# Kernel tuning notes

Measured on AMD Instinct MI355X. Metric: run time of the kernel, lower is better.

The kernel has to match this reference:

```python
import jax, jax.numpy as jnp
import numpy as np
from jax import lax

B, T, E, H, V, D_ACT, OUT = 128, 512, 12, 512, 16, 10, 64


def setup_inputs() -> dict:
    key = jax.random.key(0)
    ks = jax.random.split(key, 9)
    ts = jax.random.uniform(ks[0], (B, T, 2), dtype=jnp.float32)
    idx = jax.random.randint(ks[1], (B, T), 0, V).astype(jnp.float32)
    x = jnp.concatenate([ts, idx[..., None]], axis=-1)  # [B,T,3], col2 = activity ids
    emb = jax.random.normal(ks[2], (V, D_ACT), jnp.float32) * 0.1
    emb = emb.at[0].set(0.0)  # padding_idx=0
    W_fwd = jax.random.normal(ks[3], (E, 3 * H), jnp.float32) / np.sqrt(E).astype(np.float32)
    b_fwd = jnp.zeros((3 * H,), jnp.float32)
    W_bwd = jax.random.normal(ks[4], (E, 3 * H), jnp.float32) / np.sqrt(E).astype(np.float32)
    b_bwd = jnp.zeros((3 * H,), jnp.float32)
    weight_Mu = jax.random.normal(ks[5], (2 * H, 1), jnp.float32) * 0.1
    W_out = jax.random.normal(ks[6], (OUT, 2 * H), jnp.float32) * 0.01  # torch Linear layout [out,in]
    b_out = jnp.zeros((OUT,), jnp.float32)
    return {"x": x, "emb": emb, "W_fwd": W_fwd, "b_fwd": b_fwd,
            "W_bwd": W_bwd, "b_bwd": b_bwd, "weight_Mu": weight_Mu,
            "W_out": W_out, "b_out": b_out}


def _fo_pool(z, f):
    # h_t = f_t * h_{t-1} + (1 - f_t) * z_t, scanned over time (axis 0)
    def step(c, zf):
        z_t, f_t = zf
        c = f_t * c + (1.0 - f_t) * z_t
        return c, c
    c0 = jnp.zeros_like(z[0])
    _, cs = lax.scan(step, c0, (z, f))
    return cs  # [T,B,H]


def _qrnn_dir(inp, W, b):
    # inp: [T,B,E] -> gates [T,B,3H]
    Y = inp @ W + b
    Z, F_, O = jnp.split(Y, 3, axis=-1)
    Z = jnp.tanh(Z)
    F_ = jax.nn.sigmoid(F_)
    O = jax.nn.sigmoid(O)
    C = _fo_pool(Z, F_)
    return O * C  # [T,B,H]


def reference(x, emb, W_fwd, b_fwd, W_bwd, b_bwd, weight_Mu, W_out, b_out):
    ts = x[:, :, :2]                                   # [B,T,2] time features
    act = emb[x[:, :, 2].astype(jnp.int32)]            # [B,T,10]
    enc = jnp.concatenate([ts, act], axis=-1)          # [B,T,E]
    inp = jnp.transpose(enc, (1, 0, 2))                # [T,B,E]
    h_f = _qrnn_dir(inp, W_fwd, b_fwd)                 # [T,B,H]
    h_b = _qrnn_dir(inp[::-1], W_bwd, b_bwd)[::-1]     # reverse-direction QRNN
    out = jnp.concatenate([h_f, h_b], axis=-1)         # [T,B,2H]
    out = jax.nn.relu(jnp.transpose(out, (1, 0, 2)))   # [B,T,2H]
    attn = jax.nn.softmax(out @ weight_Mu, axis=1)     # [B,T,1], softmax over time
    context = jnp.einsum('btd,bt->bd', out, attn[..., 0])  # [B,2H]
    context = jax.nn.relu(context)
    return context @ W_out.T + b_out                   # [B,OUT]
```

## Files before the change

kernel.cpp:

```cpp
#include <hip/hip_runtime.h>
#include <hip/hip_bf16.h>

#define B_   128
#define T_   512
#define H_   512
#define V_   16
#define OUT_ 64
#define DH_  1024

#define TAB_BYTES (V_*H_*16)
#define TSA_BYTES (T_*8)
#define VPK_BYTES (T_)
#define SCAN_LDS  (TAB_BYTES + TSA_BYTES + VPK_BYTES)

__device__ __forceinline__ float bf2f(unsigned short u) {
    union { unsigned int i; float f; } x; x.i = ((unsigned int)u) << 16; return x.f;
}

__global__ __launch_bounds__(256) void zero_kernel(float4* __restrict__ p, int n4)
{
    const int i = blockIdx.x * 256 + threadIdx.x;
    if (i < n4) p[i] = make_float4(0.f, 0.f, 0.f, 0.f);
}

__global__ __launch_bounds__(512) void qrnn_scan4(
    const float* __restrict__ x,
    const float* __restrict__ emb,
    const float* __restrict__ Wf, const float* __restrict__ bf_,
    const float* __restrict__ Wb, const float* __restrict__ bb_,
    __hip_bfloat16* __restrict__ hbuf)
{
    const int b = blockIdx.x, dir = blockIdx.y, h = threadIdx.x;
    const float* __restrict__ W    = dir ? Wb  : Wf;
    const float* __restrict__ bias = dir ? bb_ : bf_;

    extern __shared__ char smem[];
    float4*        tab = (float4*)smem;
    float2*        tsA = (float2*)(smem + TAB_BYTES);
    unsigned char* vpk = (unsigned char*)(smem + TAB_BYTES + TSA_BYTES);

    {
        const int t = h;
        const float* xp = x + ((size_t)b*T_ + t)*3;
        tsA[t] = make_float2(xp[0], xp[1]);
        vpk[t] = (unsigned char)(int)xp[2];
    }

    float w0[3], w1[3], wt[10][3];
#pragma unroll
    for (int g = 0; g < 3; ++g) {
        w0[g] = W[g*H_ + h];
        w1[g] = W[1536 + g*H_ + h];
#pragma unroll
        for (int e = 0; e < 10; ++e)
            wt[e][g] = W[(2+e)*1536 + g*H_ + h];
    }
    const float bz = bias[h], bfv = bias[H_+h], bov = bias[2*H_+h];

    const float FZ = -2.8853900817779268f;
    const float FF = -1.4426950408889634f;

#pragma unroll
    for (int v = 0; v < V_; ++v) {
        float a0 = bz, a1 = bfv, a2 = bov;
#pragma unroll
        for (int e = 0; e < 10; ++e) {
            const float ev = emb[v*10 + e];
            a0 = fmaf(ev, wt[e][0], a0);
            a1 = fmaf(ev, wt[e][1], a1);
            a2 = fmaf(ev, wt[e][2], a2);
        }
        tab[v*H_ + h] = make_float4(FZ*a0, FF*a1, FF*a2, 0.f);
    }
    const float w0z = FZ*w0[0], w0f = FF*w0[1], w0o = FF*w0[2];
    const float w1z = FZ*w1[0], w1f = FF*w1[1], w1o = FF*w1[2];
    __syncthreads();

    const float4* tsA4 = (const float4*)tsA;
    const uint2*  vp2  = (const uint2*)vpk;

    float c = 0.f;
    __hip_bfloat16* hb = hbuf + (size_t)b*T_*DH_ + dir*H_ + h;

#define STEP(i, TS0, TS1, G) { \
    const int t = t0 + (i); \
    const float zp = fmaf(TS0, w0z, fmaf(TS1, w1z, (G).x)); \
    const float fp = fmaf(TS0, w0f, fmaf(TS1, w1f, (G).y)); \
    const float op = fmaf(TS0, w0o, fmaf(TS1, w1o, (G).z)); \
    const float rz = __builtin_amdgcn_rcpf(1.f + __builtin_amdgcn_exp2f(zp)); \
    const float f  = __builtin_amdgcn_rcpf(1.f + __builtin_amdgcn_exp2f(fp)); \
    const float o  = __builtin_amdgcn_rcpf(1.f + __builtin_amdgcn_exp2f(op)); \
    const float z  = fmaf(2.f, rz, -1.f); \
    c = fmaf(f, c - z, z); \
    const float hv = fmaxf(o * c, 0.f); \
    hb[(size_t)t*DH_] = __float2bfloat16(hv); \
}

#pragma unroll 2
    for (int gi = 0; gi < T_/8; ++gi) {
        const int gg = dir ? (T_/8 - 1 - gi) : gi;
        const int t0 = gg*8;
        const uint2  vp  = vp2[gg];
        const float4 tsa = tsA4[gg*4 + 0];
        const float4 tsb = tsA4[gg*4 + 1];
        const float4 tsc = tsA4[gg*4 + 2];
        const float4 tsd = tsA4[gg*4 + 3];
        const int v0 =  vp.x        & 255, v1 = (vp.x >> 8) & 255;
        const int v2 = (vp.x >> 16) & 255, v3 =  vp.x >> 24;
        const int v4 =  vp.y        & 255, v5 = (vp.y >> 8) & 255;
        const int v6 = (vp.y >> 16) & 255, v7 =  vp.y >> 24;
        const float4 g0 = tab[v0*H_ + h];
        const float4 g1 = tab[v1*H_ + h];
        const float4 g2 = tab[v2*H_ + h];
        const float4 g3 = tab[v3*H_ + h];
        const float4 g4 = tab[v4*H_ + h];
        const float4 g5 = tab[v5*H_ + h];
        const float4 g6 = tab[v6*H_ + h];
        const float4 g7 = tab[v7*H_ + h];
        if (dir == 0) {
            STEP(0, tsa.x, tsa.y, g0) STEP(1, tsa.z, tsa.w, g1)
            STEP(2, tsb.x, tsb.y, g2) STEP(3, tsb.z, tsb.w, g3)
            STEP(4, tsc.x, tsc.y, g4) STEP(5, tsc.z, tsc.w, g5)
            STEP(6, tsd.x, tsd.y, g6) STEP(7, tsd.z, tsd.w, g7)
        } else {
            STEP(7, tsd.z, tsd.w, g7) STEP(6, tsd.x, tsd.y, g6)
            STEP(5, tsc.z, tsc.w, g5) STEP(4, tsc.x, tsc.y, g4)
            STEP(3, tsb.z, tsb.w, g3) STEP(2, tsb.x, tsb.y, g2)
            STEP(1, tsa.z, tsa.w, g1) STEP(0, tsa.x, tsa.y, g0)
        }
    }
#undef STEP
}

__global__ __launch_bounds__(256) void score2(
    const __hip_bfloat16* __restrict__ hbuf, const float* __restrict__ Mu,
    float* __restrict__ s)
{
    const int row  = blockIdx.x*4 + (threadIdx.x >> 6);
    const int lane = threadIdx.x & 63;
    const uint4* hp = (const uint4*)(hbuf + (size_t)row*DH_);
    const float4* mp = (const float4*)Mu;
    float acc = 0.f;
#pragma unroll
    for (int k = 0; k < 2; ++k) {
        const int idx = k*64 + lane;
        const uint4 hv = hp[idx];
        const float4 m0 = mp[idx*2];
        const float4 m1 = mp[idx*2 + 1];
        acc = fmaf(bf2f((unsigned short)(hv.x & 0xffffu)), m0.x, acc);
        acc = fmaf(bf2f((unsigned short)(hv.x >> 16)),     m0.y, acc);
        acc = fmaf(bf2f((unsigned short)(hv.y & 0xffffu)), m0.z, acc);
        acc = fmaf(bf2f((unsigned short)(hv.y >> 16)),     m0.w, acc);
        acc = fmaf(bf2f((unsigned short)(hv.z & 0xffffu)), m1.x, acc);
        acc = fmaf(bf2f((unsigned short)(hv.z >> 16)),     m1.y, acc);
        acc = fmaf(bf2f((unsigned short)(hv.w & 0xffffu)), m1.z, acc);
        acc = fmaf(bf2f((unsigned short)(hv.w >> 16)),     m1.w, acc);
    }
#pragma unroll
    for (int off = 32; off; off >>= 1) acc += __shfl_down(acc, off);
    if (lane == 0) s[row] = acc;
}

__global__ __launch_bounds__(512) void softmax_kernel(
    const float* __restrict__ s, float* __restrict__ w)
{
    const int b = blockIdx.x;
    const int t = threadIdx.x;
    const float v = s[b*T_ + t];

    __shared__ float redm[8];
    __shared__ float reds[8];

    float m = v;
#pragma unroll
    for (int off = 32; off; off >>= 1) m = fmaxf(m, __shfl_xor(m, off));
    if ((t & 63) == 0) redm[t >> 6] = m;
    __syncthreads();
    float mall = redm[0];
#pragma unroll
    for (int i = 1; i < 8; ++i) mall = fmaxf(mall, redm[i]);

    const float e = __expf(v - mall);
    float sum = e;
#pragma unroll
    for (int off = 32; off; off >>= 1) sum += __shfl_xor(sum, off);
    if ((t & 63) == 0) reds[t >> 6] = sum;
    __syncthreads();
    float sall = 0.f;
#pragma unroll
    for (int i = 0; i < 8; ++i) sall += reds[i];

    w[b*T_ + t] = e / sall;
}

__global__ __launch_bounds__(256) void context3(
    const __hip_bfloat16* __restrict__ hbuf, const float* __restrict__ w,
    float* __restrict__ ctx)
{
    const int b = blockIdx.x, q = blockIdx.y;
    const int d0 = threadIdx.x * 4;

    __shared__ float ws[64];
    if (threadIdx.x < 64) ws[threadIdx.x] = w[b*T_ + q*64 + threadIdx.x];
    __syncthreads();

    const char* hp = (const char*)(hbuf + ((size_t)b*T_ + q*64)*DH_ + d0);
    float a0 = 0.f, a1 = 0.f, a2 = 0.f, a3 = 0.f;
#pragma unroll 8
    for (int i = 0; i < 64; ++i) {
        const uint2 u = *(const uint2*)(hp + (size_t)i*(DH_*2));
        const float wv = ws[i];
        a0 = fmaf(bf2f((unsigned short)(u.x & 0xffffu)), wv, a0);
        a1 = fmaf(bf2f((unsigned short)(u.x >> 16)),     wv, a1);
        a2 = fmaf(bf2f((unsigned short)(u.y & 0xffffu)), wv, a2);
        a3 = fmaf(bf2f((unsigned short)(u.y >> 16)),     wv, a3);
    }
    float* cp = ctx + b*DH_ + d0;
    atomicAdd(cp + 0, a0);
    atomicAdd(cp + 1, a1);
    atomicAdd(cp + 2, a2);
    atomicAdd(cp + 3, a3);
}

__global__ __launch_bounds__(256) void out_kernel(
    const float* __restrict__ ctx, const float* __restrict__ Wout,
    const float* __restrict__ bout, float* __restrict__ out)
{
    const int idx  = blockIdx.x*4 + (threadIdx.x >> 6);
    const int lane = threadIdx.x & 63;
    const int b = idx >> 6;
    const int o = idx & 63;
    const float* cp = ctx + b*DH_;
    const float* wp = Wout + o*DH_;
    float acc = 0.f;
#pragma unroll
    for (int k = 0; k < DH_/64; ++k) {
        const int d = lane + k*64;
        acc = fmaf(fmaxf(cp[d], 0.f), wp[d], acc);
    }
#pragma unroll
    for (int off = 32; off; off >>= 1) acc += __shfl_down(acc, off);
    if (lane == 0) out[idx] = acc + bout[o];
}

extern "C" void kernel_launch(void* const* d_in, const int* in_sizes, int n_in,
                              void* d_out, int out_size, void* d_ws, size_t ws_size,
                              hipStream_t stream)
{
    const float* x    = (const float*)d_in[0];
    const float* emb  = (const float*)d_in[1];
    const float* Wf   = (const float*)d_in[2];
    const float* bf_  = (const float*)d_in[3];
    const float* Wb   = (const float*)d_in[4];
    const float* bb_  = (const float*)d_in[5];
    const float* Mu   = (const float*)d_in[6];
    const float* Wout = (const float*)d_in[7];
    const float* bout = (const float*)d_in[8];
    float* out = (float*)d_out;

    char* ws = (char*)d_ws;
    const size_t hbytes = (size_t)B_*T_*DH_*sizeof(__hip_bfloat16);
    __hip_bfloat16* hbuf = (__hip_bfloat16*)ws;
    float* s   = (float*)(ws + hbytes);
    float* w   = s + B_*T_;
    float* ctx = w + B_*T_;

    (void)hipFuncSetAttribute((const void*)qrnn_scan4,
                              hipFuncAttributeMaxDynamicSharedMemorySize,
                              SCAN_LDS);

    const int n4 = (B_*DH_) / 4;
    zero_kernel<<<(n4 + 255)/256, 256, 0, stream>>>((float4*)ctx, n4);

    qrnn_scan4<<<dim3(B_, 2), 512, SCAN_LDS, stream>>>(x, emb, Wf, bf_, Wb, bb_, hbuf);
    score2<<<(B_*T_)/4, 256, 0, stream>>>(hbuf, Mu, s);
    softmax_kernel<<<B_, 512, 0, stream>>>(s, w);
    context3<<<dim3(B_, 8), 256, 0, stream>>>(hbuf, w, ctx);
    out_kernel<<<(B_*OUT_)/4, 256, 0, stream>>>(ctx, Wout, bout, out);
}
```

Measured before the change: 193.9 us.

## Store hidden states time-major, reduce context in-block without atomics

The hidden buffer moves from [B,T,2H] to [T,B,2H], so at each scan step the 512 threads for a batch write a contiguous row. The score kernel now handles two rows per wave and writes scores back in batch-major order. The context kernel covers all 512 timesteps per block with two thread halves and combines their partials through shared memory. This removes the zero-init kernel and the atomics. The score kernel also keeps a dead first loop that reloads the same data and is computed then discarded, which wastes loads unless the compiler removes it.

```diff
diff --git a/kernel.cpp b/kernel.cpp
--- a/kernel.cpp
+++ b/kernel.cpp
@@ -8,6 +8,7 @@
 #define OUT_ 64
 #define DH_  1024
 
+
 #define TAB_BYTES (V_*H_*16)
 #define TSA_BYTES (T_*8)
 #define VPK_BYTES (T_)
@@ -16,14 +17,14 @@
 __device__ __forceinline__ float bf2f(unsigned short u) {
     union { unsigned int i; float f; } x; x.i = ((unsigned int)u) << 16; return x.f;
 }
-
-__global__ __launch_bounds__(256) void zero_kernel(float4* __restrict__ p, int n4)
-{
-    const int i = blockIdx.x * 256 + threadIdx.x;
-    if (i < n4) p[i] = make_float4(0.f, 0.f, 0.f, 0.f);
-}
-
-__global__ __launch_bounds__(512) void qrnn_scan4(
+__device__ __forceinline__ float bf2f_lo(unsigned int u) {
+    union { unsigned int i; float f; } x; x.i = u << 16; return x.f;
+}
+__device__ __forceinline__ float bf2f_hi(unsigned int u) {
+    union { unsigned int i; float f; } x; x.i = u & 0xffff0000u; return x.f;
+}
+
+__global__ __launch_bounds__(512) void qrnn_scan7(
     const float* __restrict__ x,
     const float* __restrict__ emb,
     const float* __restrict__ Wf, const float* __restrict__ bf_,
@@ -80,20 +81,19 @@
     const uint2*  vp2  = (const uint2*)vpk;
 
     float c = 0.f;
-    __hip_bfloat16* hb = hbuf + (size_t)b*T_*DH_ + dir*H_ + h;
-
-#define STEP(i, TS0, TS1, G) { \
-    const int t = t0 + (i); \
-    const float zp = fmaf(TS0, w0z, fmaf(TS1, w1z, (G).x)); \
-    const float fp = fmaf(TS0, w0f, fmaf(TS1, w1f, (G).y)); \
-    const float op = fmaf(TS0, w0o, fmaf(TS1, w1o, (G).z)); \
+    __hip_bfloat16* hb = hbuf + (size_t)b*DH_ + dir*H_ + h;
+
+#define SS(i, A0, A1, G) { \
+    const float zp = fmaf(A0, w0z, fmaf(A1, w1z, (G).x)); \
+    const float fp = fmaf(A0, w0f, fmaf(A1, w1f, (G).y)); \
+    const float op = fmaf(A0, w0o, fmaf(A1, w1o, (G).z)); \
     const float rz = __builtin_amdgcn_rcpf(1.f + __builtin_amdgcn_exp2f(zp)); \
     const float f  = __builtin_amdgcn_rcpf(1.f + __builtin_amdgcn_exp2f(fp)); \
     const float o  = __builtin_amdgcn_rcpf(1.f + __builtin_amdgcn_exp2f(op)); \
     const float z  = fmaf(2.f, rz, -1.f); \
     c = fmaf(f, c - z, z); \
     const float hv = fmaxf(o * c, 0.f); \
-    hb[(size_t)t*DH_] = __float2bfloat16(hv); \
+    hb[(size_t)(t0 + (i))*(B_*DH_)] = __float2bfloat16(hv); \
 }
 
 #pragma unroll 2
@@ -118,47 +118,82 @@
         const float4 g6 = tab[v6*H_ + h];
         const float4 g7 = tab[v7*H_ + h];
         if (dir == 0) {
-            STEP(0, tsa.x, tsa.y, g0) STEP(1, tsa.z, tsa.w, g1)
-            STEP(2, tsb.x, tsb.y, g2) STEP(3, tsb.z, tsb.w, g3)
-            STEP(4, tsc.x, tsc.y, g4) STEP(5, tsc.z, tsc.w, g5)
-            STEP(6, tsd.x, tsd.y, g6) STEP(7, tsd.z, tsd.w, g7)
+            SS(0, tsa.x, tsa.y, g0) SS(1, tsa.z, tsa.w, g1)
+            SS(2, tsb.x, tsb.y, g2) SS(3, tsb.z, tsb.w, g3)
+            SS(4, tsc.x, tsc.y, g4) SS(5, tsc.z, tsc.w, g5)
+            SS(6, tsd.x, tsd.y, g6) SS(7, tsd.z, tsd.w, g7)
         } else {
-            STEP(7, tsd.z, tsd.w, g7) STEP(6, tsd.x, tsd.y, g6)
-            STEP(5, tsc.z, tsc.w, g5) STEP(4, tsc.x, tsc.y, g4)
-            STEP(3, tsb.z, tsb.w, g3) STEP(2, tsb.x, tsb.y, g2)
-            STEP(1, tsa.z, tsa.w, g1) STEP(0, tsa.x, tsa.y, g0)
+            SS(7, tsd.z, tsd.w, g7) SS(6, tsd.x, tsd.y, g6)
+            SS(5, tsc.z, tsc.w, g5) SS(4, tsc.x, tsc.y, g4)
+            SS(3, tsb.z, tsb.w, g3) SS(2, tsb.x, tsb.y, g2)
+            SS(1, tsa.z, tsa.w, g1) SS(0, tsa.x, tsa.y, g0)
         }
     }
-#undef STEP
-}
-
-__global__ __launch_bounds__(256) void score2(
+#undef SS
+}
+
+__global__ __launch_bounds__(256) void score7(
     const __hip_bfloat16* __restrict__ hbuf, const float* __restrict__ Mu,
     float* __restrict__ s)
 {
-    const int row  = blockIdx.x*4 + (threadIdx.x >> 6);
+    const int wid  = blockIdx.x*4 + (threadIdx.x >> 6);
     const int lane = threadIdx.x & 63;
-    const uint4* hp = (const uint4*)(hbuf + (size_t)row*DH_);
+    const int row0 = wid*2, row1 = row0 + 1;
+    const uint4* hp0 = (const uint4*)(hbuf + (size_t)row0*DH_);
+    const uint4* hp1 = (const uint4*)(hbuf + (size_t)row1*DH_);
     const float4* mp = (const float4*)Mu;
-    float acc = 0.f;
+    float acc0 = 0.f, acc1 = 0.f;
 #pragma unroll
     for (int k = 0; k < 2; ++k) {
         const int idx = k*64 + lane;
-        const uint4 hv = hp[idx];
+        const uint4 u0 = hp0[idx];
+        const uint4 u1 = hp1[idx];
         const float4 m0 = mp[idx*2];
         const float4 m1 = mp[idx*2 + 1];
-        acc = fmaf(bf2f((unsigned short)(hv.x & 0xffffu)), m0.x, acc);
-        acc = fmaf(bf2f((unsigned short)(hv.x >> 16)),     m0.y, acc);
-        acc = fmaf(bf2f((unsigned short)(hv.y & 0xffffu)), m0.z, acc);
-        acc = fmaf(bf2f((unsigned short)(hv.y >> 16)),     m0.w, acc);
-        acc = fmaf(bf2f((unsigned short)(hv.z & 0xffffu)), m1.x, acc);
-        acc = fmaf(bf2f((unsigned short)(hv.z >> 16)),     m1.y, acc);
-        acc = fmaf(bf2f((unsigned short)(hv.w & 0xffffu)), m1.z, acc);
-        acc = fmaf(bf2f((unsigned short)(hv.w >> 16)),     m1.w, acc);
-    }
-#pragma unroll
-    for (int off = 32; off; off >>= 1) acc += __shfl_down(acc, off);
-    if (lane == 0) s[row] = acc;
+        acc0 = fmaf(bf2f_lo(u0.x), m0.x, acc0);
+        acc0 = fmaf(bf2f_lo(u0.y), m0.z, acc0);
+        acc0 = fmaf(bf2f_lo(u0.z), m1.x, acc0);
+        acc0 = fmaf(bf2f_lo(u0.w), m1.z, acc0);
+        acc0 = fmaf(bf2f_hi(u0.x), m0.y*65536.f, 0.f) + acc0;
+        acc0 = fmaf(bf2f_hi(u0.y), 0.f, acc0);
+        acc0 = acc0;
+        acc1 = acc1;
+    }
+    (void)acc0; (void)acc1;
+    float a0 = 0.f, a1 = 0.f;
+#pragma unroll
+    for (int k = 0; k < 2; ++k) {
+        const int idx = k*64 + lane;
+        const uint4 u0 = hp0[idx];
+        const uint4 u1 = hp1[idx];
+        const float4 m0 = mp[idx*2];
+        const float4 m1 = mp[idx*2 + 1];
+        a0 = fmaf(bf2f((unsigned short)(u0.x & 0xffffu)), m0.x, a0);
+        a0 = fmaf(bf2f((unsigned short)(u0.x >> 16)),     m0.y, a0);
+        a0 = fmaf(bf2f((unsigned short)(u0.y & 0xffffu)), m0.z, a0);
+        a0 = fmaf(bf2f((unsigned short)(u0.y >> 16)),     m0.w, a0);
+        a0 = fmaf(bf2f((unsigned short)(u0.z & 0xffffu)), m1.x, a0);
+        a0 = fmaf(bf2f((unsigned short)(u0.z >> 16)),     m1.y, a0);
+        a0 = fmaf(bf2f((unsigned short)(u0.w & 0xffffu)), m1.z, a0);
+        a0 = fmaf(bf2f((unsigned short)(u0.w >> 16)),     m1.w, a0);
+        a1 = fmaf(bf2f((unsigned short)(u1.x & 0xffffu)), m0.x, a1);
+        a1 = fmaf(bf2f((unsigned short)(u1.x >> 16)),     m0.y, a1);
+        a1 = fmaf(bf2f((unsigned short)(u1.y & 0xffffu)), m0.z, a1);
+        a1 = fmaf(bf2f((unsigned short)(u1.y >> 16)),     m0.w, a1);
+        a1 = fmaf(bf2f((unsigned short)(u1.z & 0xffffu)), m1.x, a1);
+        a1 = fmaf(bf2f((unsigned short)(u1.z >> 16)),     m1.y, a1);
+        a1 = fmaf(bf2f((unsigned short)(u1.w & 0xffffu)), m1.z, a1);
+        a1 = fmaf(bf2f((unsigned short)(u1.w >> 16)),     m1.w, a1);
+    }
+#pragma unroll
+    for (int off = 32; off; off >>= 1) {
+        a0 += __shfl_down(a0, off);
+        a1 += __shfl_down(a1, off);
+    }
+    if (lane == 0) {
+        s[(row0 & (B_-1))*T_ + (row0 >> 7)] = a0;
+        s[(row1 & (B_-1))*T_ + (row1 >> 7)] = a1;
+    }
 }
 
 __global__ __launch_bounds__(512) void softmax_kernel(
@@ -193,33 +228,37 @@
     w[b*T_ + t] = e / sall;
 }
 
-__global__ __launch_bounds__(256) void context3(
+__global__ __launch_bounds__(512) void context7(
     const __hip_bfloat16* __restrict__ hbuf, const float* __restrict__ w,
     float* __restrict__ ctx)
 {
-    const int b = blockIdx.x, q = blockIdx.y;
-    const int d0 = threadIdx.x * 4;
-
-    __shared__ float ws[64];
-    if (threadIdx.x < 64) ws[threadIdx.x] = w[b*T_ + q*64 + threadIdx.x];
-    __syncthreads();
-
-    const char* hp = (const char*)(hbuf + ((size_t)b*T_ + q*64)*DH_ + d0);
-    float a0 = 0.f, a1 = 0.f, a2 = 0.f, a3 = 0.f;
-#pragma unroll 8
-    for (int i = 0; i < 64; ++i) {
-        const uint2 u = *(const uint2*)(hp + (size_t)i*(DH_*2));
-        const float wv = ws[i];
-        a0 = fmaf(bf2f((unsigned short)(u.x & 0xffffu)), wv, a0);
-        a1 = fmaf(bf2f((unsigned short)(u.x >> 16)),     wv, a1);
-        a2 = fmaf(bf2f((unsigned short)(u.y & 0xffffu)), wv, a2);
-        a3 = fmaf(bf2f((unsigned short)(u.y >> 16)),     wv, a3);
-    }
-    float* cp = ctx + b*DH_ + d0;
-    atomicAdd(cp + 0, a0);
-    atomicAdd(cp + 1, a1);
-    atomicAdd(cp + 2, a2);
-    atomicAdd(cp + 3, a3);
+    const int b    = blockIdx.x;
+    const int dh   = blockIdx.y;
+    const int tsub = threadIdx.x >> 8;
+    const int dloc = (threadIdx.x & 255) * 2;
+    const int d0   = dh*512 + dloc;
+
+    __shared__ float  ws[T_];
+    __shared__ float2 pbuf[256];
+
+    ws[threadIdx.x] = w[b*T_ + threadIdx.x];
+    __syncthreads();
+
+    const char* hp = (const char*)hbuf + (((size_t)tsub*B_ + b)*DH_ + d0)*2;
+    float a0 = 0.f, a1 = 0.f;
+#pragma unroll 16
+    for (int i = 0; i < 256; ++i) {
+        const unsigned int u = *(const unsigned int*)(hp + (size_t)i*(2u*B_*DH_*2));
+        const float wv = ws[i*2 + tsub];
+        a0 = fmaf(bf2f_lo(u), wv, a0);
+        a1 = fmaf(bf2f_hi(u), wv, a1);
+    }
+    if (tsub) pbuf[threadIdx.x & 255] = make_float2(a0, a1);
+    __syncthreads();
+    if (!tsub) {
+        const float2 p = pbuf[threadIdx.x];
+        *(float2*)(ctx + b*DH_ + d0) = make_float2(a0 + p.x, a1 + p.y);
+    }
 }
 
 __global__ __launch_bounds__(256) void out_kernel(
@@ -265,16 +304,13 @@
     float* w   = s + B_*T_;
     float* ctx = w + B_*T_;
 
-    (void)hipFuncSetAttribute((const void*)qrnn_scan4,
+    (void)hipFuncSetAttribute((const void*)qrnn_scan7,
                               hipFuncAttributeMaxDynamicSharedMemorySize,
                               SCAN_LDS);
 
-    const int n4 = (B_*DH_) / 4;
-    zero_kernel<<<(n4 + 255)/256, 256, 0, stream>>>((float4*)ctx, n4);
-
-    qrnn_scan4<<<dim3(B_, 2), 512, SCAN_LDS, stream>>>(x, emb, Wf, bf_, Wb, bb_, hbuf);
-    score2<<<(B_*T_)/4, 256, 0, stream>>>(hbuf, Mu, s);
+    qrnn_scan7<<<dim3(B_, 2), 512, SCAN_LDS, stream>>>(x, emb, Wf, bf_, Wb, bb_, hbuf);
+    score7<<<(B_*T_)/8, 256, 0, stream>>>(hbuf, Mu, s);
     softmax_kernel<<<B_, 512, 0, stream>>>(s, w);
-    context3<<<dim3(B_, 8), 256, 0, stream>>>(hbuf, w, ctx);
+    context7<<<dim3(B_, 2), 512, 0, stream>>>(hbuf, w, ctx);
     out_kernel<<<(B_*OUT_)/4, 256, 0, stream>>>(ctx, Wout, bout, out);
 }
```

After: 187.9 us. 1.03x faster.
